# Performance work log

Measured on AMD Instinct MI355X. Metric: run time of the kernel, lower is better.

## Reference

```python
import jax, jax.numpy as jnp
import numpy as np
from jax import lax

B, CIN, COUT, H, W = 4, 256, 256, 64, 64
KH = KW = 3
K = KH * KW
GN_GROUPS = 32
EPS = 1e-5


def setup_inputs() -> dict:
    key = jax.random.key(0)
    ks = jax.random.split(key, 6)
    x = jax.random.normal(ks[0], (B, CIN, H, W), jnp.float32)
    # offset predictor conv: 3x3, 18 out channels, with bias (init small so offsets stay near 0)
    offset_w = jax.random.normal(ks[1], (2 * K, CIN, KH, KW), jnp.float32) * 0.01
    offset_b = jax.random.normal(ks[2], (2 * K,), jnp.float32) * 0.01
    # deformable conv weight (no bias), He-ish scale
    deform_w = jax.random.normal(ks[3], (COUT, CIN, KH, KW), jnp.float32) * (1.0 / np.sqrt(CIN * K))
    gn_gamma = jnp.ones((COUT,), jnp.float32)
    gn_beta = jnp.zeros((COUT,), jnp.float32)
    return {"x": x, "offset_w": offset_w, "offset_b": offset_b,
            "deform_w": deform_w, "gn_gamma": gn_gamma, "gn_beta": gn_beta}


def _deform_conv(x, offset, weight):
    """Deformable conv v1, stride=1, pad=1, dil=1, deformable_groups=1.
    x: [B,C,H,W]; offset: [B,2K,H,W] with (dy,dx) per kernel tap; weight: [O,C,3,3].
    """
    b, c, h, w = x.shape
    off = offset.reshape(b, K, 2, h, w)
    # base sampling grid per kernel tap: p = p0 - pad + k
    ky, kx = jnp.meshgrid(jnp.arange(KH), jnp.arange(KW), indexing="ij")
    base_y = (jnp.arange(h, dtype=jnp.float32) - 1.0)[None, :, None] + ky.reshape(K).astype(jnp.float32)[:, None, None]  # [K,H,1]
    base_x = (jnp.arange(w, dtype=jnp.float32) - 1.0)[None, None, :] + kx.reshape(K).astype(jnp.float32)[:, None, None]  # [K,1,W]
    py = base_y[None] + off[:, :, 0]  # [B,K,H,W]
    px = base_x[None] + off[:, :, 1]  # [B,K,H,W]

    y0 = jnp.floor(py)
    x0 = jnp.floor(px)
    ty = py - y0
    tx = px - x0
    y0 = y0.astype(jnp.int32)
    x0 = x0.astype(jnp.int32)

    x_hw = x.transpose(0, 2, 3, 1).reshape(b, h * w, c)  # [B,HW,C]

    def corner(yi, xi, wgt):
        valid = (yi >= 0) & (yi < h) & (xi >= 0) & (xi < w)
        yc = jnp.clip(yi, 0, h - 1)
        xc = jnp.clip(xi, 0, w - 1)
        idx = (yc * w + xc).reshape(b, K * h * w)
        v = jnp.take_along_axis(x_hw, idx[..., None], axis=1)  # [B,KHW,C]
        return v * (wgt * valid.astype(wgt.dtype)).reshape(b, K * h * w, 1)

    samp = (corner(y0, x0, (1 - ty) * (1 - tx))
            + corner(y0, x0 + 1, (1 - ty) * tx)
            + corner(y0 + 1, x0, ty * (1 - tx))
            + corner(y0 + 1, x0 + 1, ty * tx))  # [B,KHW,C]
    samp = samp.reshape(b, K, h, w, c)
    return jnp.einsum("bkhwc,ock->bohw", samp, weight.reshape(weight.shape[0], c, K))


def reference(x, offset_w, offset_b, deform_w, gn_gamma, gn_beta):
    # offset = conv3x3(x) + bias
    offset = lax.conv_general_dilated(
        x, offset_w, window_strides=(1, 1), padding=((1, 1), (1, 1)),
        dimension_numbers=("NCHW", "OIHW", "NCHW")) + offset_b[None, :, None, None]
    out = _deform_conv(x, offset, deform_w)
    # GroupNorm(32, COUT) + ReLU
    b, c, h, w = out.shape
    g = out.reshape(b, GN_GROUPS, (c // GN_GROUPS) * h * w)
    mu = g.mean(axis=2, keepdims=True)
    var = g.var(axis=2, keepdims=True)
    g = (g - mu) * lax.rsqrt(var + EPS)
    out = g.reshape(b, c, h, w) * gn_gamma[None, :, None, None] + gn_beta[None, :, None, None]
    return jax.nn.relu(out)
```

## Files before the change

kernel.cpp:

```cpp
#include <hip/hip_runtime.h>
#include <hip/hip_bf16.h>
#include <stdint.h>


typedef unsigned short u16;
typedef __bf16 bf16x8 __attribute__((ext_vector_type(8)));
typedef float f32x4_t __attribute__((ext_vector_type(4)));

#define HW 4096

__device__ __forceinline__ uint32_t f32_to_bf16_rne(float f) {
  uint32_t u = __builtin_bit_cast(uint32_t, f);
  return (u + 0x7FFFu + ((u >> 16) & 1u)) >> 16;
}
__device__ __forceinline__ float bf_lo(uint32_t u) {
  return __builtin_bit_cast(float, u << 16);
}
__device__ __forceinline__ float bf_hi(uint32_t u) {
  return __builtin_bit_cast(float, u & 0xFFFF0000u);
}
__device__ __forceinline__ uint32_t blend2(uint32_t a, uint32_t b, uint32_t c,
                                           uint32_t d, float4 mw) {
  float lo = mw.x * bf_lo(a) + mw.y * bf_lo(b) + mw.z * bf_lo(c) + mw.w * bf_lo(d);
  float hi = mw.x * bf_hi(a) + mw.y * bf_hi(b) + mw.z * bf_hi(c) + mw.w * bf_hi(d);
  return f32_to_bf16_rne(lo) | (f32_to_bf16_rne(hi) << 16);
}

__global__ __launch_bounds__(256) void k_pre(const float* __restrict__ x,
                                             const float* __restrict__ wsrc,
                                             const float* __restrict__ ow,
                                             u16* __restrict__ xt,
                                             u16* __restrict__ warr,
                                             u16* __restrict__ owm,
                                             float* __restrict__ part) {
  __shared__ float tile[32][33];
  int bid = blockIdx.x;
  int tid = threadIdx.x;
  if (bid < 4096) {
    int bx = bid & 127, by = (bid >> 7) & 7, bz = bid >> 10;
    int c0 = by * 32, p0 = bx * 32;
    int tx = tid & 31, ty = tid >> 5;
#pragma unroll
    for (int j = 0; j < 32; j += 8)
      tile[ty + j][tx] = x[(bz * 256 + c0 + ty + j) * HW + p0 + tx];
    __syncthreads();
    int cp = tid & 15;
    int pr = tid >> 4;
#pragma unroll
    for (int j = 0; j < 2; j++) {
      int p = pr + j * 16;
      uint32_t lo = f32_to_bf16_rne(tile[cp * 2][p]);
      uint32_t hi = f32_to_bf16_rne(tile[cp * 2 + 1][p]);
      *(uint32_t*)&xt[(bz * HW + p0 + p) * 256 + c0 + cp * 2] = lo | (hi << 16);
    }
  } else if (bid < 6400) {
    int e = (bid - 4096) * 256 + tid;
    int kk = e & 7, m = (e >> 3) & 255, g = (e >> 11) & 7, kc = e >> 14;
    int cin = (kc & 3) * 64 + g * 8 + kk;
    int tap = kc >> 2;
    warr[e] = (u16)f32_to_bf16_rne(wsrc[m * 2304 + cin * 9 + tap]);
  } else if (bid < 6688) {
    int e = (bid - 6400) * 256 + tid;
    int kk = e & 7, m = (e >> 3) & 31, g = (e >> 8) & 7, kc = e >> 11;
    int cin = (kc & 3) * 64 + g * 8 + kk;
    int tap = kc >> 2;
    float v = (m < 18) ? ow[m * 2304 + cin * 9 + tap] : 0.f;
    owm[e] = (u16)f32_to_bf16_rne(v);
  } else {
    part[tid] = 0.f;
  }
}

__global__ __launch_bounds__(512, 4) void k_conv(
    const u16* __restrict__ xt, const u16* __restrict__ warr,
    const u16* __restrict__ owm, const float* __restrict__ ob,
    float* __restrict__ out, float* __restrict__ part) {
  __shared__ char smem[54272];
  u16* stage = (u16*)smem;
  float* off_part = (float*)(smem + 33792);
  int4* ci_s = (int4*)smem;
  float4* mw_s = (float4*)(smem + 4608);
  u16* b_s = (u16*)(smem + 9216);

  int tid = threadIdx.x;
  int lane = tid & 63;
  int wm = tid >> 6;
  int wk = (blockIdx.x & 7) * 64 + (blockIdx.x >> 3);
  int b = wk >> 7;
  int pt = wk & 127;
  int p0 = pt * 32;
  int yrow = p0 >> 6, xbase = p0 & 63;

  {
    u16* st = stage + wm * 2112;
    int q = lane & 15, pq = lane >> 4;
    int oct = lane & 7, pxs = lane >> 3;
    f32x4_t a2[2][2] = {};
#pragma unroll 1
    for (int kc = wm; kc < 36; kc += 8) {
      int tap = kc >> 2, cc = kc & 3;
      int ky = tap / 3, kx = tap % 3;
      int yy = yrow + ky - 1;
      bool vy = (yy >= 0) && (yy < 64);
#pragma unroll
      for (int i = 0; i < 4; i++) {
        int px = i * 8 + pxs;
        int xx2 = xbase + px + kx - 1;
        uint4 v = make_uint4(0u, 0u, 0u, 0u);
        if (vy && xx2 >= 0 && xx2 < 64)
          v = *(const uint4*)&xt[(b * HW + yy * 64 + xx2) * 256 + cc * 64 + oct * 8];
        *(uint4*)&st[oct * 264 + px * 8] = v;
      }
#pragma unroll
      for (int ks = 0; ks < 2; ks++) {
        int g = ks * 4 + pq;
        const u16* ab = owm + kc * 2048 + g * 256;
#pragma unroll
        for (int s = 0; s < 2; s++) {
          bf16x8 bfr = *(bf16x8*)&st[g * 264 + (s * 16 + q) * 8];
#pragma unroll
          for (int im = 0; im < 2; im++) {
            bf16x8 af = *(const bf16x8*)&ab[(im * 16 + q) * 8];
            a2[s][im] = __builtin_amdgcn_mfma_f32_16x16x32_bf16(af, bfr, a2[s][im], 0, 0, 0);
          }
        }
      }
    }
#pragma unroll
    for (int s = 0; s < 2; s++)
#pragma unroll
      for (int im = 0; im < 2; im++)
#pragma unroll
        for (int r = 0; r < 4; r++) {
          int oc = im * 16 + pq * 4 + r;
          if (oc < 18) off_part[(wm * 32 + s * 16 + q) * 20 + oc] = a2[s][im][r];
        }
  }
  __syncthreads();
  for (int it = tid; it < 288; it += 512) {
    int tap = it >> 5;
    int px = it & 31;
    float dy = ob[2 * tap], dx = ob[2 * tap + 1];
#pragma unroll
    for (int wv = 0; wv < 8; wv++) {
      dy += off_part[(wv * 32 + px) * 20 + 2 * tap];
      dx += off_part[(wv * 32 + px) * 20 + 2 * tap + 1];
    }
    int ky = tap / 3, kx = tap % 3;
    int p = p0 + px;
    int yq = p >> 6, xq = p & 63;
    float py = (float)(yq - 1 + ky) + dy;
    float pxx = (float)(xq - 1 + kx) + dx;
    float y0f = floorf(py), x0f = floorf(pxx);
    float ty = py - y0f, tx = pxx - x0f;
    int y0 = (int)y0f, x0 = (int)x0f;
    int y1 = y0 + 1, x1 = x0 + 1;
    float wy0 = 1.f - ty, wy1 = ty, wx0 = 1.f - tx, wx1 = tx;
    bool vy0 = (y0 >= 0) && (y0 < 64), vy1 = (y1 >= 0) && (y1 < 64);
    bool vx0 = (x0 >= 0) && (x0 < 64), vx1 = (x1 >= 0) && (x1 < 64);
    int cy0 = min(max(y0, 0), 63), cy1 = min(max(y1, 0), 63);
    int cx0 = min(max(x0, 0), 63), cx1 = min(max(x1, 0), 63);
    int base = b * HW;
    int4 ci;
    ci.x = (base + cy0 * 64 + cx0) * 256;
    ci.y = (base + cy0 * 64 + cx1) * 256;
    ci.z = (base + cy1 * 64 + cx0) * 256;
    ci.w = (base + cy1 * 64 + cx1) * 256;
    float4 mw;
    mw.x = wy0 * wx0 * ((vy0 && vx0) ? 1.f : 0.f);
    mw.y = wy0 * wx1 * ((vy0 && vx1) ? 1.f : 0.f);
    mw.z = wy1 * wx0 * ((vy1 && vx0) ? 1.f : 0.f);
    mw.w = wy1 * wx1 * ((vy1 && vx1) ? 1.f : 0.f);
    ci_s[it] = ci;
    mw_s[it] = mw;
  }
  __syncthreads();

  {
    int oct8 = tid & 15;
    int pxg = tid >> 4;
    int sub = pxg >> 4;
    int pxw = pxg & 15;
    int col = lane & 15;
    int pq = lane >> 4;
    int e0 = oct8 * 8;
    f32x4_t acc[2][2] = {};

    auto stage_b = [&](uint4 c0, uint4 c1, uint4 c2, uint4 c3, float4 mw, u16* bb) {
      uint4 u;
      u.x = blend2(c0.x, c1.x, c2.x, c3.x, mw);
      u.y = blend2(c0.y, c1.y, c2.y, c3.y, mw);
      u.z = blend2(c0.z, c1.z, c2.z, c3.z, mw);
      u.w = blend2(c0.w, c1.w, c2.w, c3.w, mw);
      *(uint4*)&bb[sub * 2176 + oct8 * 136 + pxw * 8] = u;
    };
    auto gemm = [&](const u16* bb, int kcbase) {
      __builtin_amdgcn_s_setprio(1);
#pragma unroll
      for (int ks = 0; ks < 4; ks++) {
        int ro = ks * 4 + pq;
        bf16x8 bb0 = *(bf16x8*)&bb[ro * 136 + col * 8];
        bf16x8 bb1 = *(bf16x8*)&bb[2176 + ro * 136 + col * 8];
        int kc = kcbase + (ks >> 1);
        int gg = (ks & 1) * 4 + pq;
        const u16* ab = warr + kc * 16384 + gg * 2048 + (wm * 32 + col) * 8;
#pragma unroll
        for (int im = 0; im < 2; im++) {
          bf16x8 af = *(const bf16x8*)&ab[im * 128];
          acc[0][im] = __builtin_amdgcn_mfma_f32_16x16x32_bf16(af, bb0, acc[0][im], 0, 0, 0);
          acc[1][im] = __builtin_amdgcn_mfma_f32_16x16x32_bf16(af, bb1, acc[1][im], 0, 0, 0);
        }
      }
      __builtin_amdgcn_s_setprio(0);
    };

    int4 ci0 = ci_s[pxg];
    float4 mw_cur = mw_s[pxg];
    uint4 a0 = *(const uint4*)&xt[ci0.x + e0];
    uint4 a1 = *(const uint4*)&xt[ci0.y + e0];
    uint4 a2v = *(const uint4*)&xt[ci0.z + e0];
    uint4 a3 = *(const uint4*)&xt[ci0.w + e0];
    uint4 g0 = *(const uint4*)&xt[ci0.x + 128 + e0];
    uint4 g1 = *(const uint4*)&xt[ci0.y + 128 + e0];
    uint4 g2 = *(const uint4*)&xt[ci0.z + 128 + e0];
    uint4 g3 = *(const uint4*)&xt[ci0.w + 128 + e0];
    float4 mw_nxt = mw_cur;
    int4 ci_n = ci0;

#pragma unroll 1
    for (int dp = 0; dp < 9; dp++) {
      stage_b(a0, a1, a2v, a3, mw_cur, b_s);
      __syncthreads();
      if (dp < 8) {
        ci_n = ci_s[(dp + 1) * 32 + pxg];
        mw_nxt = mw_s[(dp + 1) * 32 + pxg];
        a0 = *(const uint4*)&xt[ci_n.x + e0];
        a1 = *(const uint4*)&xt[ci_n.y + e0];
        a2v = *(const uint4*)&xt[ci_n.z + e0];
        a3 = *(const uint4*)&xt[ci_n.w + e0];
      }
      gemm(b_s, dp * 4);
      stage_b(g0, g1, g2, g3, mw_cur, b_s + 4352);
      __syncthreads();
      if (dp < 8) {
        g0 = *(const uint4*)&xt[ci_n.x + 128 + e0];
        g1 = *(const uint4*)&xt[ci_n.y + 128 + e0];
        g2 = *(const uint4*)&xt[ci_n.z + 128 + e0];
        g3 = *(const uint4*)&xt[ci_n.w + 128 + e0];
      }
      gemm(b_s + 4352, dp * 4 + 2);
      mw_cur = mw_nxt;
    }

#pragma unroll
    for (int im = 0; im < 2; im++) {
      float s = 0.f, ss = 0.f;
#pragma unroll
      for (int sb = 0; sb < 2; sb++) {
        int n = p0 + sb * 16 + col;
#pragma unroll
        for (int r = 0; r < 4; r++) {
          int m = wm * 32 + im * 16 + pq * 4 + r;
          float v = acc[sb][im][r];
          out[(b * 256 + m) * HW + n] = v;
          s += v;
          ss += v * v;
        }
      }
#pragma unroll
      for (int msk = 1; msk <= 16; msk <<= 1) {
        s += __shfl_xor(s, msk);
        ss += __shfl_xor(ss, msk);
      }
      if ((lane & 31) == 0) {
        int grp = wm * 4 + im * 2 + (lane >> 5);
        float* pp = part + (b * 32 + grp) * 2;
        atomicAdd(pp, s);
        atomicAdd(pp + 1, ss);
      }
    }
  }
}

__global__ __launch_bounds__(256) void k_gn_apply(float* __restrict__ out,
                                                  const float2* __restrict__ part,
                                                  const float* __restrict__ gamma,
                                                  const float* __restrict__ beta) {
  int gid = blockIdx.x * 256 + threadIdx.x;
  int c = (gid >> 10) & 255;
  int bb = gid >> 18;
  float2 p = part[bb * 32 + (c >> 3)];
  float mu = p.x / 32768.f;
  float var = p.y / 32768.f - mu * mu;
  float rs = rsqrtf(var + 1e-5f);
  float ga = gamma[c] * rs;
  float be = beta[c] - mu * ga;
  float4 v = ((const float4*)out)[gid];
  v.x = fmaxf(v.x * ga + be, 0.f);
  v.y = fmaxf(v.y * ga + be, 0.f);
  v.z = fmaxf(v.z * ga + be, 0.f);
  v.w = fmaxf(v.w * ga + be, 0.f);
  ((float4*)out)[gid] = v;
}

extern "C" void kernel_launch(void* const* d_in, const int* in_sizes, int n_in,
                              void* d_out, int out_size, void* d_ws, size_t ws_size,
                              hipStream_t stream) {
  const float* x = (const float*)d_in[0];
  const float* offset_w = (const float*)d_in[1];
  const float* offset_b = (const float*)d_in[2];
  const float* deform_w = (const float*)d_in[3];
  const float* gn_gamma = (const float*)d_in[4];
  const float* gn_beta = (const float*)d_in[5];
  float* out = (float*)d_out;
  char* ws = (char*)d_ws;

  u16* xt = (u16*)ws;
  u16* warr = (u16*)(ws + 8388608);
  u16* owm = (u16*)(ws + 9568256);
  float* part = (float*)(ws + 9715712);

  k_pre<<<dim3(6689), dim3(256), 0, stream>>>(x, deform_w, offset_w, xt, warr, owm, part);
  k_conv<<<dim3(512), dim3(512), 0, stream>>>(xt, warr, owm, offset_b, out, part);
  k_gn_apply<<<dim3(4096), dim3(256), 0, stream>>>(out, (const float2*)part, gn_gamma, gn_beta);
}
```

Baseline: 157.7 us.

## Double-buffer blended B tiles to halve barriers per deformable tap

Restructures the per-tap loop so that both channel halves are blended and written to shared memory before a single barrier. The staging buffer now alternates between two halves selected by tap parity, which removes the second __syncthreads per iteration. All eight gathers for the next tap are issued together ahead of an 8-step MFMA loop. This trades fewer barriers and longer MFMA runs for more live registers and double the shared-memory footprint for the B tile, and it relies on b_s being sized for two buffers.

```diff
diff --git a/kernel.cpp b/kernel.cpp
--- a/kernel.cpp
+++ b/kernel.cpp
@@ -186,22 +186,59 @@
     int e0 = oct8 * 8;
     f32x4_t acc[2][2] = {};
 
-    auto stage_b = [&](uint4 c0, uint4 c1, uint4 c2, uint4 c3, float4 mw, u16* bb) {
-      uint4 u;
-      u.x = blend2(c0.x, c1.x, c2.x, c3.x, mw);
-      u.y = blend2(c0.y, c1.y, c2.y, c3.y, mw);
-      u.z = blend2(c0.z, c1.z, c2.z, c3.z, mw);
-      u.w = blend2(c0.w, c1.w, c2.w, c3.w, mw);
-      *(uint4*)&bb[sub * 2176 + oct8 * 136 + pxw * 8] = u;
-    };
-    auto gemm = [&](const u16* bb, int kcbase) {
+    int4 ci = ci_s[pxg];
+    float4 mw = mw_s[pxg];
+    uint4 A0 = *(const uint4*)&xt[ci.x + e0];
+    uint4 A1 = *(const uint4*)&xt[ci.y + e0];
+    uint4 A2 = *(const uint4*)&xt[ci.z + e0];
+    uint4 A3 = *(const uint4*)&xt[ci.w + e0];
+    uint4 G0 = *(const uint4*)&xt[ci.x + 128 + e0];
+    uint4 G1 = *(const uint4*)&xt[ci.y + 128 + e0];
+    uint4 G2 = *(const uint4*)&xt[ci.z + 128 + e0];
+    uint4 G3 = *(const uint4*)&xt[ci.w + 128 + e0];
+
+#pragma unroll 1
+    for (int dp = 0; dp < 9; dp++) {
+      u16* bb = b_s + (dp & 1) * 8704;
+      {
+        uint4 u;
+        u.x = blend2(A0.x, A1.x, A2.x, A3.x, mw);
+        u.y = blend2(A0.y, A1.y, A2.y, A3.y, mw);
+        u.z = blend2(A0.z, A1.z, A2.z, A3.z, mw);
+        u.w = blend2(A0.w, A1.w, A2.w, A3.w, mw);
+        *(uint4*)&bb[sub * 2176 + oct8 * 136 + pxw * 8] = u;
+      }
+      {
+        uint4 v;
+        v.x = blend2(G0.x, G1.x, G2.x, G3.x, mw);
+        v.y = blend2(G0.y, G1.y, G2.y, G3.y, mw);
+        v.z = blend2(G0.z, G1.z, G2.z, G3.z, mw);
+        v.w = blend2(G0.w, G1.w, G2.w, G3.w, mw);
+        *(uint4*)&bb[4352 + sub * 2176 + oct8 * 136 + pxw * 8] = v;
+      }
+      __syncthreads();
+      if (dp < 8) {
+        ci = ci_s[(dp + 1) * 32 + pxg];
+        float4 mwn = mw_s[(dp + 1) * 32 + pxg];
+        A0 = *(const uint4*)&xt[ci.x + e0];
+        A1 = *(const uint4*)&xt[ci.y + e0];
+        A2 = *(const uint4*)&xt[ci.z + e0];
+        A3 = *(const uint4*)&xt[ci.w + e0];
+        G0 = *(const uint4*)&xt[ci.x + 128 + e0];
+        G1 = *(const uint4*)&xt[ci.y + 128 + e0];
+        G2 = *(const uint4*)&xt[ci.z + 128 + e0];
+        G3 = *(const uint4*)&xt[ci.w + 128 + e0];
+        mw = mwn;
+      }
       __builtin_amdgcn_s_setprio(1);
 #pragma unroll
-      for (int ks = 0; ks < 4; ks++) {
-        int ro = ks * 4 + pq;
-        bf16x8 bb0 = *(bf16x8*)&bb[ro * 136 + col * 8];
-        bf16x8 bb1 = *(bf16x8*)&bb[2176 + ro * 136 + col * 8];
-        int kc = kcbase + (ks >> 1);
+      for (int ks = 0; ks < 8; ks++) {
+        int set = ks >> 2;
+        int ro = (ks & 3) * 4 + pq;
+        const u16* bp = bb + set * 4352 + ro * 136 + col * 8;
+        bf16x8 bb0 = *(const bf16x8*)&bp[0];
+        bf16x8 bb1 = *(const bf16x8*)&bp[2176];
+        int kc = dp * 4 + (ks >> 1);
         int gg = (ks & 1) * 4 + pq;
         const u16* ab = warr + kc * 16384 + gg * 2048 + (wm * 32 + col) * 8;
 #pragma unroll
@@ -212,44 +249,6 @@
         }
       }
       __builtin_amdgcn_s_setprio(0);
-    };
-
-    int4 ci0 = ci_s[pxg];
-    float4 mw_cur = mw_s[pxg];
-    uint4 a0 = *(const uint4*)&xt[ci0.x + e0];
-    uint4 a1 = *(const uint4*)&xt[ci0.y + e0];
-    uint4 a2v = *(const uint4*)&xt[ci0.z + e0];
-    uint4 a3 = *(const uint4*)&xt[ci0.w + e0];
-    uint4 g0 = *(const uint4*)&xt[ci0.x + 128 + e0];
-    uint4 g1 = *(const uint4*)&xt[ci0.y + 128 + e0];
-    uint4 g2 = *(const uint4*)&xt[ci0.z + 128 + e0];
-    uint4 g3 = *(const uint4*)&xt[ci0.w + 128 + e0];
-    float4 mw_nxt = mw_cur;
-    int4 ci_n = ci0;
-
-#pragma unroll 1
-    for (int dp = 0; dp < 9; dp++) {
-      stage_b(a0, a1, a2v, a3, mw_cur, b_s);
-      __syncthreads();
-      if (dp < 8) {
-        ci_n = ci_s[(dp + 1) * 32 + pxg];
-        mw_nxt = mw_s[(dp + 1) * 32 + pxg];
-        a0 = *(const uint4*)&xt[ci_n.x + e0];
-        a1 = *(const uint4*)&xt[ci_n.y + e0];
-        a2v = *(const uint4*)&xt[ci_n.z + e0];
-        a3 = *(const uint4*)&xt[ci_n.w + e0];
-      }
-      gemm(b_s, dp * 4);
-      stage_b(g0, g1, g2, g3, mw_cur, b_s + 4352);
-      __syncthreads();
-      if (dp < 8) {
-        g0 = *(const uint4*)&xt[ci_n.x + 128 + e0];
-        g1 = *(const uint4*)&xt[ci_n.y + 128 + e0];
-        g2 = *(const uint4*)&xt[ci_n.z + 128 + e0];
-        g3 = *(const uint4*)&xt[ci_n.w + 128 + e0];
-      }
-      gemm(b_s + 4352, dp * 4 + 2);
-      mw_cur = mw_nxt;
     }
 
 #pragma unroll
```

Result: no change. 154.8 us (median of 2 runs) (-1.8%).
